# Kernel tuning notes

Hardware: AMD Instinct MI355X
Metric: run time of the kernel (lower is better)

## Reference

```python
import jax, jax.numpy as jnp
import numpy as np

H = 512  # hidden_size
A = 1.0  # hard_sigm slope


def hard_sigm(a, x):
    return jnp.clip((a * x + 1.0) / 2.0, 0.0, 1.0)


def setup_inputs() -> dict:
    key = jax.random.key(0)
    ks = jax.random.split(key, 10)
    B = 8192
    bottom, top = 512, 512
    stdv = 1.0 / np.sqrt(H)
    u = lambda k, shp: jax.random.uniform(k, shp, jnp.float32, -stdv, stdv)
    return {
        "c": jax.random.normal(ks[0], (H, B), jnp.float32),
        "h_bottom": jax.random.normal(ks[1], (bottom, B), jnp.float32),
        "h": jax.random.normal(ks[2], (H, B), jnp.float32),
        "h_top": jax.random.normal(ks[3], (top, B), jnp.float32),
        "z": jax.random.uniform(ks[4], (1, B), jnp.float32),
        "z_bottom": jax.random.uniform(ks[5], (1, B), jnp.float32),
        "U_11": u(ks[6], (4 * H + 1, H)),
        "U_21": u(ks[7], (4 * H + 1, top)),
        "W_01": u(ks[8], (4 * H + 1, bottom)),
        "bias": u(ks[9], (4 * H + 1,)),
    }


def reference(c, h_bottom, h, h_top, z, z_bottom, U_11, U_21, W_01, bias):
    # z, z_bottom: (1, B) boundary indicators broadcast over the gate axis
    s_recur = (1.0 - z) * (U_11 @ h)          # (4H+1, B)
    s_topdown = z * (U_21 @ h_top)            # last_layer=False
    s_bottomup = z_bottom * (W_01 @ h_bottom)
    f_s = s_recur + s_topdown + s_bottomup + bias[:, None]

    f = jax.nn.sigmoid(f_s[0:H, :])
    i = jax.nn.sigmoid(f_s[H:2 * H, :])
    o = jax.nn.sigmoid(f_s[2 * H:3 * H, :])
    g = jnp.tanh(f_s[3 * H:4 * H, :])
    z_hat = hard_sigm(A, f_s[4 * H:4 * H + 1, :])  # (1, B)

    ig = i * g
    c_new = z * ig + (1.0 - z) * (1.0 - z_bottom) * c \
        + (1.0 - z) * z_bottom * (f * c + ig)
    tanh_c = jnp.tanh(c_new)
    h_new = z * o * tanh_c + (1.0 - z) * (1.0 - z_bottom) * h \
        + (1.0 - z) * z_bottom * o * tanh_c
    return (h_new, c_new, z_hat)
```

## Files before the change

### kernel.cpp

```cpp
#include <hip/hip_runtime.h>
#include <hip/hip_bf16.h>

#define HH 512
#define BB 8192
#define KK 1536
#define NT 48
#define HB 4194304
#define BLOB 8192

typedef __bf16 bhalf;
typedef __bf16 bf16x8 __attribute__((ext_vector_type(8)));
typedef float  f32x4  __attribute__((ext_vector_type(4)));

typedef __attribute__((address_space(1))) void* as1_t;
typedef __attribute__((address_space(3))) void* as3_t;

#define GLDS(src, dst) __builtin_amdgcn_global_load_lds((as1_t)(void*)(src), (as3_t)(void*)(dst), 16, 0, 0)
#define SBAR() asm volatile("s_barrier" ::: "memory")
#define VM8()  asm volatile("s_waitcnt vmcnt(8)" ::: "memory")
#define VM6()  asm volatile("s_waitcnt vmcnt(6)" ::: "memory")
#define VM4()  asm volatile("s_waitcnt vmcnt(4)" ::: "memory")
#define VM0()  asm volatile("s_waitcnt vmcnt(0)" ::: "memory")


__global__ __launch_bounds__(256) void prep_x(
    const float* __restrict__ h, const float* __restrict__ ht,
    const float* __restrict__ hb, const float* __restrict__ z,
    const float* __restrict__ zb, bhalf* __restrict__ XtP)
{
    __shared__ float tile[32][257];
    const int tid = threadIdx.x;
    const int kt  = blockIdx.x;
    const int nt  = blockIdx.y;
    const int n   = nt * 256 + tid;
    const int kb  = kt * 32;

    const float* src; int kr; float scale;
    if (kb < 512)       { src = h;  kr = kb;        scale = 1.f - z[n]; }
    else if (kb < 1024) { src = ht; kr = kb - 512;  scale = z[n]; }
    else                { src = hb; kr = kb - 1024; scale = zb[n]; }

    #pragma unroll
    for (int kk = 0; kk < 32; ++kk)
        tile[kk][tid] = src[(size_t)(kr + kk) * BB + n] * scale;
    __syncthreads();

    bhalf* blob = XtP + (size_t)(nt * NT + kt) * BLOB;
    #pragma unroll
    for (int q = 0; q < 4; ++q) {
        const int s  = q * 256 + tid;
        const int rb = s >> 6, w = s & 63;
        const int hh = w >> 4, lrr = w & 15;
        const int nloc = rb * 16 + lrr, kloc = hh * 8;
        bf16x8 r;
        #pragma unroll
        for (int e = 0; e < 8; ++e) r[e] = (bhalf)tile[kloc + e][nloc];
        *(bf16x8*)(blob + s * 8) = r;
    }
}

__global__ __launch_bounds__(256) void prep_w(
    const float* __restrict__ U11, const float* __restrict__ U21,
    const float* __restrict__ W01, bhalf* __restrict__ WcP)
{
    const int o    = blockIdx.x * 4 + (threadIdx.x >> 6);
    const int lane = threadIdx.x & 63;
    const int g = o >> 9, j = o & 511;
    const int mp = 4 * j + g;
    const int mt = mp >> 8, rb = (mp >> 4) & 15, lrr = mp & 15;

    #pragma unroll
    for (int p = 0; p < 3; ++p) {
        const float* src = (p == 0) ? U11 : (p == 1) ? U21 : W01;
        const float* rp  = src + (size_t)o * 512 + lane * 8;
        float4 v0 = *(const float4*)rp;
        float4 v1 = *(const float4*)(rp + 4);
        bf16x8 r;
        r[0]=(bhalf)v0.x; r[1]=(bhalf)v0.y; r[2]=(bhalf)v0.z; r[3]=(bhalf)v0.w;
        r[4]=(bhalf)v1.x; r[5]=(bhalf)v1.y; r[6]=(bhalf)v1.z; r[7]=(bhalf)v1.w;
        const int kt = p * 16 + (lane >> 2);
        const int hh = lane & 3;
        *(bf16x8*)(WcP + (size_t)(mt * NT + kt) * BLOB
                   + rb * 512 + hh * 128 + lrr * 8) = r;
    }
}

__device__ __forceinline__ float sigmf(float x)    { return 1.f / (1.f + __expf(-x)); }
__device__ __forceinline__ float tanhfast(float x) { return 2.f / (1.f + __expf(-2.f * x)) - 1.f; }

__global__ __launch_bounds__(512, 2) void gemm_fused(
    const bhalf* __restrict__ WcP, const bhalf* __restrict__ XtP,
    const float* __restrict__ bias, const float* __restrict__ c_in,
    const float* __restrict__ h_in, const float* __restrict__ z,
    const float* __restrict__ zb, float* __restrict__ out)
{
    __shared__ bhalf As[4][BLOB];
    __shared__ bhalf Bs[4][BLOB];

    const int tid  = threadIdx.x;
    const int lane = tid & 63;
    const int wid  = tid >> 6;
    const int wm   = wid >> 2, wn = wid & 3;
    const int lr   = lane & 15, hi = lane >> 4;
    const int soff = hi * 128 + lr * 8;

    const int xcd = blockIdx.x & 7;
    const int i   = blockIdx.x >> 3;
    const int mt  = i & 7;
    const int nt  = xcd * 4 + (i >> 3);
    const int m0 = mt * 256, n0 = nt * 256;

    const bhalf* gA = WcP + (size_t)mt * (NT * BLOB) + tid * 8;
    const bhalf* gB = XtP + (size_t)nt * (NT * BLOB) + tid * 8;

    const bhalf* pA0 = &As[0][wm * 4096 + soff];
    const bhalf* pA1 = &As[1][wm * 4096 + soff];
    const bhalf* pA2 = &As[2][wm * 4096 + soff];
    const bhalf* pA3 = &As[3][wm * 4096 + soff];
    const bhalf* pB0 = &Bs[0][wn * 2048 + soff];
    const bhalf* pB1 = &Bs[1][wn * 2048 + soff];
    const bhalf* pB2 = &Bs[2][wn * 2048 + soff];
    const bhalf* pB3 = &Bs[3][wn * 2048 + soff];

#define STAGE_A(t, bf) do { const bhalf* s_ = gA + (size_t)(t) * BLOB;        \
        GLDS(s_, &As[bf][tid * 8]); GLDS(s_ + 4096, &As[bf][tid * 8 + 4096]); } while (0)
#define STAGE_B(t, bf) do { const bhalf* s_ = gB + (size_t)(t) * BLOB;        \
        GLDS(s_, &Bs[bf][tid * 8]); GLDS(s_ + 4096, &Bs[bf][tid * 8 + 4096]); } while (0)

#define RDA(bf, i_) (*(const bf16x8*)(pA##bf + (i_) * 512))
#define RDB(bf, i_) (*(const bf16x8*)(pB##bf + (i_) * 512))

#define MF(mi, ni, A_, B_) acc[mi][ni] = \
    __builtin_amdgcn_mfma_f32_16x16x32_bf16(A_, B_, acc[mi][ni], 0, 0, 0)

#define CL_LO(B0,B1,B2,B3) do { __builtin_amdgcn_s_setprio(1);                \
    MF(0,0,aL0,B0); MF(0,1,aL0,B1); MF(0,2,aL0,B2); MF(0,3,aL0,B3);           \
    MF(1,0,aL1,B0); MF(1,1,aL1,B1); MF(1,2,aL1,B2); MF(1,3,aL1,B3);           \
    MF(2,0,aL2,B0); MF(2,1,aL2,B1); MF(2,2,aL2,B2); MF(2,3,aL2,B3);           \
    MF(3,0,aL3,B0); MF(3,1,aL3,B1); MF(3,2,aL3,B2); MF(3,3,aL3,B3);           \
    __builtin_amdgcn_s_setprio(0); } while (0)

#define CL_HI(B0,B1,B2,B3) do { __builtin_amdgcn_s_setprio(1);                \
    MF(4,0,aH0,B0); MF(4,1,aH0,B1); MF(4,2,aH0,B2); MF(4,3,aH0,B3);           \
    MF(5,0,aH1,B0); MF(5,1,aH1,B1); MF(5,2,aH1,B2); MF(5,3,aH1,B3);           \
    MF(6,0,aH2,B0); MF(6,1,aH2,B1); MF(6,2,aH2,B2); MF(6,3,aH2,B3);           \
    MF(7,0,aH3,B0); MF(7,1,aH3,B1); MF(7,2,aH3,B2); MF(7,3,aH3,B3);           \
    __builtin_amdgcn_s_setprio(0); } while (0)

#define PH0(bfc, tst, bfst, DOST, B0,B1,B2,B3) do {                           \
    aH0 = RDA(bfc,4); aH1 = RDA(bfc,5); aH2 = RDA(bfc,6); aH3 = RDA(bfc,7);   \
    if (DOST) STAGE_A(tst, bfst);                                             \
    SBAR(); CL_LO(B0,B1,B2,B3); SBAR(); } while (0)

#define PH1(bfn, tst, bfst, DOST, DORD, VMW, B0,B1,B2,B3, N0,N1,N2,N3) do {   \
    VMW;                                                                      \
    if (DORD) { N0 = RDB(bfn,0); N1 = RDB(bfn,1); N2 = RDB(bfn,2);            \
                N3 = RDB(bfn,3);                                              \
                aL0 = RDA(bfn,0); aL1 = RDA(bfn,1); aL2 = RDA(bfn,2);         \
                aL3 = RDA(bfn,3); }                                           \
    if (DOST) STAGE_B(tst, bfst);                                             \
    SBAR(); CL_HI(B0,B1,B2,B3); SBAR(); } while (0)

    f32x4 acc[8][4] = {};
    bf16x8 aL0, aL1, aL2, aL3, aH0, aH1, aH2, aH3;
    bf16x8 bA0, bA1, bA2, bA3, bB0, bB1, bB2, bB3;

    STAGE_A(0, 0); STAGE_B(0, 0);
    STAGE_A(1, 1); STAGE_B(1, 1);
    STAGE_A(2, 2); STAGE_B(2, 2);
    VM8(); SBAR();
    bA0 = RDB(0,0); bA1 = RDB(0,1); bA2 = RDB(0,2); bA3 = RDB(0,3);
    aL0 = RDA(0,0); aL1 = RDA(0,1); aL2 = RDA(0,2); aL3 = RDA(0,3);

#define QUAD(base) do {                                                       \
    PH0(0, (base)+3, 3, 1, bA0,bA1,bA2,bA3);                                  \
    PH1(1, (base)+3, 3, 1, 1, VM6(), bA0,bA1,bA2,bA3, bB0,bB1,bB2,bB3);       \
    PH0(1, (base)+4, 0, 1, bB0,bB1,bB2,bB3);                                  \
    PH1(2, (base)+4, 0, 1, 1, VM6(), bB0,bB1,bB2,bB3, bA0,bA1,bA2,bA3);       \
    PH0(2, (base)+5, 1, 1, bA0,bA1,bA2,bA3);                                  \
    PH1(3, (base)+5, 1, 1, 1, VM6(), bA0,bA1,bA2,bA3, bB0,bB1,bB2,bB3);       \
    PH0(3, (base)+6, 2, 1, bB0,bB1,bB2,bB3);                                  \
    PH1(0, (base)+6, 2, 1, 1, VM6(), bB0,bB1,bB2,bB3, bA0,bA1,bA2,bA3);       \
} while (0)

    for (int base = 0; base < 44; base += 4) {
        QUAD(base);
    }
    PH0(0, 47, 3, 1, bA0,bA1,bA2,bA3);
    PH1(1, 47, 3, 1, 1, VM6(), bA0,bA1,bA2,bA3, bB0,bB1,bB2,bB3);
    PH0(1, 0, 0, 0, bB0,bB1,bB2,bB3);
    PH1(2, 0, 0, 0, 1, VM4(), bB0,bB1,bB2,bB3, bA0,bA1,bA2,bA3);
    PH0(2, 0, 0, 0, bA0,bA1,bA2,bA3);
    PH1(3, 0, 0, 0, 1, VM0(), bA0,bA1,bA2,bA3, bB0,bB1,bB2,bB3);
    PH0(3, 0, 0, 0, bB0,bB1,bB2,bB3);
    PH1(0, 0, 0, 0, 0, ((void)0), bB0,bB1,bB2,bB3, bA0,bA1,bA2,bA3);

    const int colbase = n0 + wn * 64 + lr;
    float zc[4], zbc[4];
    #pragma unroll
    for (int ni = 0; ni < 4; ++ni) {
        zc[ni]  = z[colbase + ni * 16];
        zbc[ni] = zb[colbase + ni * 16];
    }
    #pragma unroll
    for (int mi = 0; mi < 8; ++mi) {
        const int j = (m0 >> 2) + wm * 32 + mi * 4 + hi;
        const float bf_ = bias[j];
        const float bi_ = bias[512 + j];
        const float bo_ = bias[1024 + j];
        const float bg_ = bias[1536 + j];
        #pragma unroll
        for (int ni = 0; ni < 4; ++ni) {
            const int col = colbase + ni * 16;
            const size_t idx = (size_t)j * BB + col;
            const float cv = c_in[idx];
            const float hv = h_in[idx];
            const float fv = sigmf(acc[mi][ni][0] + bf_);
            const float iv = sigmf(acc[mi][ni][1] + bi_);
            const float ov = sigmf(acc[mi][ni][2] + bo_);
            const float gv = tanhfast(acc[mi][ni][3] + bg_);
            const float ig = iv * gv;
            const float zq = zc[ni], zbq = zbc[ni];
            const float cn = zq * ig + (1.f - zq) * (1.f - zbq) * cv
                           + (1.f - zq) * zbq * (fv * cv + ig);
            const float tc = tanhfast(cn);
            const float hn = (zq + (1.f - zq) * zbq) * ov * tc
                           + (1.f - zq) * (1.f - zbq) * hv;
            out[idx]      = hn;
            out[HB + idx] = cn;
        }
    }
}

__global__ __launch_bounds__(256) void zhat_k(
    const bhalf* __restrict__ XtP, const float* __restrict__ U11,
    const float* __restrict__ U21, const float* __restrict__ W01,
    const float* __restrict__ bias, float* __restrict__ out)
{
    __shared__ float wlds[1536];
    __shared__ float red[8][32];
    const int tid = threadIdx.x;
    for (int idx = tid; idx < 1536; idx += 256) {
        float v;
        if (idx < 512)       v = U11[1048576 + idx];
        else if (idx < 1024) v = U21[1048576 + idx - 512];
        else                 v = W01[1048576 + idx - 1024];
        wlds[idx] = v;
    }
    __syncthreads();

    const int col = tid & 31, kg = tid >> 5;
    const int n = blockIdx.x * 32 + col;
    const int nt = n >> 8, rb = (n >> 4) & 15, lrr = n & 15;
    const bhalf* base = XtP + (size_t)nt * (NT * BLOB) + rb * 512;

    float acc = 0.f;
    for (int kt = kg * 6; kt < kg * 6 + 6; ++kt) {
        #pragma unroll
        for (int hh = 0; hh < 4; ++hh) {
            bf16x8 v = *(const bf16x8*)(base + (size_t)kt * BLOB + hh * 128 + lrr * 8);
            #pragma unroll
            for (int e = 0; e < 8; ++e)
                acc += (float)v[e] * wlds[kt * 32 + hh * 8 + e];
        }
    }
    red[kg][col] = acc;
    __syncthreads();
    if (tid < 32) {
        float s = 0.f;
        #pragma unroll
        for (int k2 = 0; k2 < 8; ++k2) s += red[k2][tid];
        const float v = (s + bias[2048] + 1.f) * 0.5f;
        out[(size_t)2 * HB + blockIdx.x * 32 + tid] = fminf(fmaxf(v, 0.f), 1.f);
    }
}

extern "C" void kernel_launch(void* const* d_in, const int* in_sizes, int n_in,
                              void* d_out, int out_size, void* d_ws, size_t ws_size,
                              hipStream_t stream) {
    const float* c    = (const float*)d_in[0];
    const float* hb   = (const float*)d_in[1];
    const float* h    = (const float*)d_in[2];
    const float* ht   = (const float*)d_in[3];
    const float* z    = (const float*)d_in[4];
    const float* zb   = (const float*)d_in[5];
    const float* U11  = (const float*)d_in[6];
    const float* U21  = (const float*)d_in[7];
    const float* W01  = (const float*)d_in[8];
    const float* bias = (const float*)d_in[9];
    float* out = (float*)d_out;

    char* ws = (char*)d_ws;
    bhalf* XtP = (bhalf*)ws;
    bhalf* WcP = (bhalf*)(ws + 25165824);

    prep_x    <<<dim3(48, 32), 256, 0, stream>>>(h, ht, hb, z, zb, XtP);
    prep_w    <<<512, 256, 0, stream>>>(U11, U21, W01, WcP);
    gemm_fused<<<256, 512, 0, stream>>>(WcP, XtP, bias, c, h, z, zb, out);
    zhat_k    <<<256, 256, 0, stream>>>(XtP, U11, U21, W01, bias, out);
}
```

Baseline: 85.37 us.

## Replace two-phase ping-pong GEMM schedule with single-barrier-per-tile pipeline

Drops the half-tile ping-pong schedule, where A and B stage issues, register prefetch of the next tile's fragments and two barriers per half were interleaved. It is replaced by a simpler loop: wait for the oldest tile, one barrier, issue the combined A+B global-to-LDS stage three tiles ahead, then read all A/B fragments from LDS and run 32 MFMAs. The aim is to cut barrier count and scheduling overhead. The cost is that LDS fragment loads are no longer overlapped with the previous tile's MFMAs, and the wave-interleaving priority pattern is lost.

```diff
diff --git a/kernel.cpp b/kernel.cpp
--- a/kernel.cpp
+++ b/kernel.cpp
@@ -18,7 +18,6 @@
 #define GLDS(src, dst) __builtin_amdgcn_global_load_lds((as1_t)(void*)(src), (as3_t)(void*)(dst), 16, 0, 0)
 #define SBAR() asm volatile("s_barrier" ::: "memory")
 #define VM8()  asm volatile("s_waitcnt vmcnt(8)" ::: "memory")
-#define VM6()  asm volatile("s_waitcnt vmcnt(6)" ::: "memory")
 #define VM4()  asm volatile("s_waitcnt vmcnt(4)" ::: "memory")
 #define VM0()  asm volatile("s_waitcnt vmcnt(0)" ::: "memory")
 
@@ -122,78 +121,55 @@
     const bhalf* pB2 = &Bs[2][wn * 2048 + soff];
     const bhalf* pB3 = &Bs[3][wn * 2048 + soff];
 
-#define STAGE_A(t, bf) do { const bhalf* s_ = gA + (size_t)(t) * BLOB;        \
-        GLDS(s_, &As[bf][tid * 8]); GLDS(s_ + 4096, &As[bf][tid * 8 + 4096]); } while (0)
-#define STAGE_B(t, bf) do { const bhalf* s_ = gB + (size_t)(t) * BLOB;        \
-        GLDS(s_, &Bs[bf][tid * 8]); GLDS(s_ + 4096, &Bs[bf][tid * 8 + 4096]); } while (0)
-
-#define RDA(bf, i_) (*(const bf16x8*)(pA##bf + (i_) * 512))
-#define RDB(bf, i_) (*(const bf16x8*)(pB##bf + (i_) * 512))
+#define STAGE(t, bf) do {                                                     \
+        const bhalf* sa_ = gA + (size_t)(t) * BLOB;                           \
+        const bhalf* sb_ = gB + (size_t)(t) * BLOB;                           \
+        GLDS(sa_, &As[bf][tid * 8]); GLDS(sa_ + 4096, &As[bf][tid * 8 + 4096]); \
+        GLDS(sb_, &Bs[bf][tid * 8]); GLDS(sb_ + 4096, &Bs[bf][tid * 8 + 4096]); \
+    } while (0)
 
 #define MF(mi, ni, A_, B_) acc[mi][ni] = \
     __builtin_amdgcn_mfma_f32_16x16x32_bf16(A_, B_, acc[mi][ni], 0, 0, 0)
 
-#define CL_LO(B0,B1,B2,B3) do { __builtin_amdgcn_s_setprio(1);                \
-    MF(0,0,aL0,B0); MF(0,1,aL0,B1); MF(0,2,aL0,B2); MF(0,3,aL0,B3);           \
-    MF(1,0,aL1,B0); MF(1,1,aL1,B1); MF(1,2,aL1,B2); MF(1,3,aL1,B3);           \
-    MF(2,0,aL2,B0); MF(2,1,aL2,B1); MF(2,2,aL2,B2); MF(2,3,aL2,B3);           \
-    MF(3,0,aL3,B0); MF(3,1,aL3,B1); MF(3,2,aL3,B2); MF(3,3,aL3,B3);           \
-    __builtin_amdgcn_s_setprio(0); } while (0)
-
-#define CL_HI(B0,B1,B2,B3) do { __builtin_amdgcn_s_setprio(1);                \
-    MF(4,0,aH0,B0); MF(4,1,aH0,B1); MF(4,2,aH0,B2); MF(4,3,aH0,B3);           \
-    MF(5,0,aH1,B0); MF(5,1,aH1,B1); MF(5,2,aH1,B2); MF(5,3,aH1,B3);           \
-    MF(6,0,aH2,B0); MF(6,1,aH2,B1); MF(6,2,aH2,B2); MF(6,3,aH2,B3);           \
-    MF(7,0,aH3,B0); MF(7,1,aH3,B1); MF(7,2,aH3,B2); MF(7,3,aH3,B3);           \
-    __builtin_amdgcn_s_setprio(0); } while (0)
-
-#define PH0(bfc, tst, bfst, DOST, B0,B1,B2,B3) do {                           \
-    aH0 = RDA(bfc,4); aH1 = RDA(bfc,5); aH2 = RDA(bfc,6); aH3 = RDA(bfc,7);   \
-    if (DOST) STAGE_A(tst, bfst);                                             \
-    SBAR(); CL_LO(B0,B1,B2,B3); SBAR(); } while (0)
-
-#define PH1(bfn, tst, bfst, DOST, DORD, VMW, B0,B1,B2,B3, N0,N1,N2,N3) do {   \
-    VMW;                                                                      \
-    if (DORD) { N0 = RDB(bfn,0); N1 = RDB(bfn,1); N2 = RDB(bfn,2);            \
-                N3 = RDB(bfn,3);                                              \
-                aL0 = RDA(bfn,0); aL1 = RDA(bfn,1); aL2 = RDA(bfn,2);         \
-                aL3 = RDA(bfn,3); }                                           \
-    if (DOST) STAGE_B(tst, bfst);                                             \
-    SBAR(); CL_HI(B0,B1,B2,B3); SBAR(); } while (0)
+#define CT(q) do {                                                            \
+    bf16x8 b0 = *(const bf16x8*)(pB##q);                                      \
+    bf16x8 b1 = *(const bf16x8*)(pB##q + 512);                                \
+    bf16x8 b2 = *(const bf16x8*)(pB##q + 1024);                               \
+    bf16x8 b3 = *(const bf16x8*)(pB##q + 1536);                               \
+    bf16x8 a0 = *(const bf16x8*)(pA##q);                                      \
+    bf16x8 a1 = *(const bf16x8*)(pA##q + 512);                                \
+    bf16x8 a2 = *(const bf16x8*)(pA##q + 1024);                               \
+    bf16x8 a3 = *(const bf16x8*)(pA##q + 1536);                               \
+    bf16x8 a4 = *(const bf16x8*)(pA##q + 2048);                               \
+    bf16x8 a5 = *(const bf16x8*)(pA##q + 2560);                               \
+    bf16x8 a6 = *(const bf16x8*)(pA##q + 3072);                               \
+    bf16x8 a7 = *(const bf16x8*)(pA##q + 3584);                               \
+    __builtin_amdgcn_s_setprio(1);                                            \
+    MF(0,0,a0,b0); MF(0,1,a0,b1); MF(0,2,a0,b2); MF(0,3,a0,b3);               \
+    MF(1,0,a1,b0); MF(1,1,a1,b1); MF(1,2,a1,b2); MF(1,3,a1,b3);               \
+    MF(2,0,a2,b0); MF(2,1,a2,b1); MF(2,2,a2,b2); MF(2,3,a2,b3);               \
+    MF(3,0,a3,b0); MF(3,1,a3,b1); MF(3,2,a3,b2); MF(3,3,a3,b3);               \
+    MF(4,0,a4,b0); MF(4,1,a4,b1); MF(4,2,a4,b2); MF(4,3,a4,b3);               \
+    MF(5,0,a5,b0); MF(5,1,a5,b1); MF(5,2,a5,b2); MF(5,3,a5,b3);               \
+    MF(6,0,a6,b0); MF(6,1,a6,b1); MF(6,2,a6,b2); MF(6,3,a6,b3);               \
+    MF(7,0,a7,b0); MF(7,1,a7,b1); MF(7,2,a7,b2); MF(7,3,a7,b3);               \
+    __builtin_amdgcn_s_setprio(0);                                            \
+} while (0)
 
     f32x4 acc[8][4] = {};
-    bf16x8 aL0, aL1, aL2, aL3, aH0, aH1, aH2, aH3;
-    bf16x8 bA0, bA1, bA2, bA3, bB0, bB1, bB2, bB3;
-
-    STAGE_A(0, 0); STAGE_B(0, 0);
-    STAGE_A(1, 1); STAGE_B(1, 1);
-    STAGE_A(2, 2); STAGE_B(2, 2);
-    VM8(); SBAR();
-    bA0 = RDB(0,0); bA1 = RDB(0,1); bA2 = RDB(0,2); bA3 = RDB(0,3);
-    aL0 = RDA(0,0); aL1 = RDA(0,1); aL2 = RDA(0,2); aL3 = RDA(0,3);
-
-#define QUAD(base) do {                                                       \
-    PH0(0, (base)+3, 3, 1, bA0,bA1,bA2,bA3);                                  \
-    PH1(1, (base)+3, 3, 1, 1, VM6(), bA0,bA1,bA2,bA3, bB0,bB1,bB2,bB3);       \
-    PH0(1, (base)+4, 0, 1, bB0,bB1,bB2,bB3);                                  \
-    PH1(2, (base)+4, 0, 1, 1, VM6(), bB0,bB1,bB2,bB3, bA0,bA1,bA2,bA3);       \
-    PH0(2, (base)+5, 1, 1, bA0,bA1,bA2,bA3);                                  \
-    PH1(3, (base)+5, 1, 1, 1, VM6(), bA0,bA1,bA2,bA3, bB0,bB1,bB2,bB3);       \
-    PH0(3, (base)+6, 2, 1, bB0,bB1,bB2,bB3);                                  \
-    PH1(0, (base)+6, 2, 1, 1, VM6(), bB0,bB1,bB2,bB3, bA0,bA1,bA2,bA3);       \
-} while (0)
+
+    STAGE(0, 0); STAGE(1, 1); STAGE(2, 2);
 
     for (int base = 0; base < 44; base += 4) {
-        QUAD(base);
-    }
-    PH0(0, 47, 3, 1, bA0,bA1,bA2,bA3);
-    PH1(1, 47, 3, 1, 1, VM6(), bA0,bA1,bA2,bA3, bB0,bB1,bB2,bB3);
-    PH0(1, 0, 0, 0, bB0,bB1,bB2,bB3);
-    PH1(2, 0, 0, 0, 1, VM4(), bB0,bB1,bB2,bB3, bA0,bA1,bA2,bA3);
-    PH0(2, 0, 0, 0, bA0,bA1,bA2,bA3);
-    PH1(3, 0, 0, 0, 1, VM0(), bA0,bA1,bA2,bA3, bB0,bB1,bB2,bB3);
-    PH0(3, 0, 0, 0, bB0,bB1,bB2,bB3);
-    PH1(0, 0, 0, 0, 0, ((void)0), bB0,bB1,bB2,bB3, bA0,bA1,bA2,bA3);
+        VM8(); SBAR(); STAGE(base + 3, 3); CT(0);
+        VM8(); SBAR(); STAGE(base + 4, 0); CT(1);
+        VM8(); SBAR(); STAGE(base + 5, 1); CT(2);
+        VM8(); SBAR(); STAGE(base + 6, 2); CT(3);
+    }
+    VM8(); SBAR(); STAGE(47, 3); CT(0);
+    VM8(); SBAR(); CT(1);
+    VM4(); SBAR(); CT(2);
+    VM0(); SBAR(); CT(3);
 
     const int colbase = n0 + wn * 64 + lr;
     float zc[4], zbc[4];
```

Result: faster. 82.19 us (-3.7%).
